# Kernel optimization log

Hardware: AMD Instinct MI355X
Metric: run time of the kernel (lower is better)

The kernel has to match this reference:

```python
import jax, jax.numpy as jnp
import numpy as np

NUM_HEADS = 16
DIM_MODEL = 1024
DIM_K = DIM_MODEL // NUM_HEADS  # 64


def setup_inputs() -> dict:
    key = jax.random.key(0)
    ks = jax.random.split(key, 8)
    B, S, D = 2, 2048, DIM_MODEL
    scale = 1.0 / np.sqrt(D)
    return {
        "X_q": jax.random.normal(ks[0], (B, S, D), dtype=jnp.float32),
        "X_k": jax.random.normal(ks[1], (B, S, D), dtype=jnp.float32),
        "X_v": jax.random.normal(ks[2], (B, S, D), dtype=jnp.float32),
        # weights stored as [in, out] (apply as x @ W)
        "W_query": jax.random.normal(ks[3], (D, D), dtype=jnp.float32) * scale,
        "W_key": jax.random.normal(ks[4], (D, D), dtype=jnp.float32) * scale,
        "W_value": jax.random.normal(ks[5], (D, D), dtype=jnp.float32) * scale,
        "W_hidden": jax.random.normal(ks[6], (D, D), dtype=jnp.float32) * scale,
        "b_hidden": jnp.zeros((D,), dtype=jnp.float32),
    }


def _split_heads(x, B, S):
    # [B, S, D] -> [B, H, S, dk]
    return x.reshape(B, S, NUM_HEADS, DIM_K).transpose(0, 2, 1, 3)


def reference(X_q, X_k, X_v, W_query, W_key, W_value, W_hidden, b_hidden):
    B, S, D = X_q.shape
    Q = _split_heads(X_q @ W_query, B, S)
    K = _split_heads(X_k @ W_key, B, X_k.shape[1])
    V = _split_heads(X_v @ W_value, B, X_v.shape[1])
    Q = Q / np.sqrt(DIM_K).astype(np.float32)
    scores = jnp.einsum("bhqd,bhkd->bhqk", Q, K)
    A = jax.nn.sigmoid(scores)  # sigmoid attention, not softmax
    H = jnp.einsum("bhqk,bhkd->bhqd", A, V)
    # group heads: [B, H, S, dk] -> [B, S, D]
    H_cat = H.transpose(0, 2, 1, 3).reshape(B, S, D)
    H_out = H_cat @ W_hidden + b_hidden
    return (H_out, A)
```

## Files before the change

### kernel.cpp

```cpp
#include <hip/hip_runtime.h>
#include <hip/hip_bf16.h>
#include <cstddef>

typedef __bf16 bf16x8 __attribute__((ext_vector_type(8)));
typedef __bf16 bf16x4 __attribute__((ext_vector_type(4)));
typedef float f32x4 __attribute__((ext_vector_type(4)));

#define MFMA16(a, b, c) __builtin_amdgcn_mfma_f32_16x16x32_bf16((a), (b), (c), 0, 0, 0)

__global__ __launch_bounds__(256) void cvt3(const float* __restrict__ a,
                                            const float* __restrict__ b,
                                            const float* __restrict__ c,
                                            __bf16* __restrict__ oa,
                                            __bf16* __restrict__ ob,
                                            __bf16* __restrict__ oc) {
  const float* src = blockIdx.y == 0 ? a : (blockIdx.y == 1 ? b : c);
  __bf16* dst = blockIdx.y == 0 ? oa : (blockIdx.y == 1 ? ob : oc);
  const size_t i = ((size_t)blockIdx.x * 256 + threadIdx.x) * 4;
  float4 v = *(const float4*)(src + i);
  bf16x4 o = {(__bf16)v.x, (__bf16)v.y, (__bf16)v.z, (__bf16)v.w};
  *(bf16x4*)(dst + i) = o;
}

__global__ __launch_bounds__(256) void twt(const float* __restrict__ w0, const float* __restrict__ w1,
                                           const float* __restrict__ w2, const float* __restrict__ w3,
                                           __bf16* __restrict__ o0, __bf16* __restrict__ o1,
                                           __bf16* __restrict__ o2, __bf16* __restrict__ o3) {
  const float* W;
  __bf16* O;
  switch (blockIdx.z) {
    case 0: W = w0; O = o0; break;
    case 1: W = w1; O = o1; break;
    case 2: W = w2; O = o2; break;
    default: W = w3; O = o3; break;
  }
  __shared__ float t[32][33];
  const int tx = threadIdx.x & 31, ty = threadIdx.x >> 5;
  const int bx = blockIdx.x * 32, by = blockIdx.y * 32;
#pragma unroll
  for (int i = 0; i < 4; ++i)
    t[ty + 8 * i][tx] = W[(size_t)(by + ty + 8 * i) * 1024 + bx + tx];
  __syncthreads();
#pragma unroll
  for (int i = 0; i < 4; ++i)
    O[(size_t)(bx + ty + 8 * i) * 1024 + by + tx] = (__bf16)t[tx][ty + 8 * i];
}

template <bool OUT_BF16>
__device__ __forceinline__ void gemm64_body(const __bf16* __restrict__ A,
                                            const __bf16* __restrict__ B,
                                            void* __restrict__ Cout,
                                            const float* __restrict__ bias,
                                            float scale) {
  constexpr int K = 1024, N = 1024;
  const int tid = threadIdx.x, wave = tid >> 6, lane = tid & 63;
  const int qd = lane >> 4, ln = lane & 15;
  const int m0 = blockIdx.y * 64, n0 = blockIdx.x * 128;
  const int wr = wave & 1, wc = wave >> 1;

  __shared__ __align__(16) __bf16 sA[64][72];
  __shared__ __align__(16) __bf16 sB[128][72];

  f32x4 acc[2][4] = {};

  const int sr = tid >> 2, sc = (tid & 3) * 8;

  for (int k0 = 0; k0 < K; k0 += 64) {
    __syncthreads();
    *(bf16x8*)&sA[sr][sc]      = *(const bf16x8*)(A + (size_t)(m0 + sr) * K + k0 + sc);
    *(bf16x8*)&sA[sr][sc + 32] = *(const bf16x8*)(A + (size_t)(m0 + sr) * K + k0 + sc + 32);
#pragma unroll
    for (int h = 0; h < 128; h += 64)
#pragma unroll
      for (int c = 0; c < 64; c += 32)
        *(bf16x8*)&sB[sr + h][sc + c] =
            *(const bf16x8*)(B + (size_t)(n0 + sr + h) * K + k0 + sc + c);
    __syncthreads();

#pragma unroll
    for (int ks = 0; ks < 64; ks += 32) {
      bf16x8 af[2], bfv[4];
#pragma unroll
      for (int i = 0; i < 2; ++i) af[i] = *(const bf16x8*)&sA[wr * 32 + i * 16 + ln][ks + qd * 8];
#pragma unroll
      for (int j = 0; j < 4; ++j) bfv[j] = *(const bf16x8*)&sB[wc * 64 + j * 16 + ln][ks + qd * 8];
#pragma unroll
      for (int i = 0; i < 2; ++i)
#pragma unroll
        for (int j = 0; j < 4; ++j) acc[i][j] = MFMA16(af[i], bfv[j], acc[i][j]);
    }
  }

#pragma unroll
  for (int i = 0; i < 2; ++i)
#pragma unroll
    for (int j = 0; j < 4; ++j)
#pragma unroll
      for (int r = 0; r < 4; ++r) {
        const int row = m0 + wr * 32 + i * 16 + qd * 4 + r;
        const int col = n0 + wc * 64 + j * 16 + ln;
        float v = acc[i][j][r] * scale;
        if (bias) v += bias[col];
        if (OUT_BF16)
          ((__bf16*)Cout)[(size_t)row * N + col] = (__bf16)v;
        else
          ((float*)Cout)[(size_t)row * N + col] = v;
      }
}

__global__ __launch_bounds__(256) void gemm_qkv(const __bf16* __restrict__ Xq,
                                                const __bf16* __restrict__ Xk,
                                                const __bf16* __restrict__ Xv,
                                                const __bf16* __restrict__ WqT,
                                                const __bf16* __restrict__ WkT,
                                                const __bf16* __restrict__ WvT,
                                                __bf16* __restrict__ Qb,
                                                __bf16* __restrict__ Kb,
                                                __bf16* __restrict__ Vb) {
  const __bf16 *A, *B;
  __bf16* O;
  float sc;
  switch (blockIdx.z) {
    case 0: A = Xq; B = WqT; O = Qb; sc = 0.125f; break;
    case 1: A = Xk; B = WkT; O = Kb; sc = 1.0f; break;
    default: A = Xv; B = WvT; O = Vb; sc = 1.0f; break;
  }
  gemm64_body<true>(A, B, (void*)O, nullptr, sc);
}

__global__ __launch_bounds__(256) void gemm_h(const __bf16* __restrict__ Hc,
                                              const __bf16* __restrict__ WhT,
                                              float* __restrict__ Hout,
                                              const float* __restrict__ bh) {
  gemm64_body<false>(Hc, WhT, (void*)Hout, bh, 1.0f);
}

__global__ __launch_bounds__(256) void attn(const __bf16* __restrict__ Q,
                                            const __bf16* __restrict__ Kb,
                                            const __bf16* __restrict__ Vb,
                                            float* __restrict__ Aout,
                                            __bf16* __restrict__ Hc) {
  const int qt = blockIdx.x, h = blockIdx.y, b = blockIdx.z;
  const int tid = threadIdx.x, wave = tid >> 6, lane = tid & 63;
  const int qd = lane >> 4, ln = lane & 15;
  const int q0 = qt * 64;
  const int wr = wave >> 1, wc = wave & 1;

  __shared__ __align__(16) __bf16 sVt[64][132];
  __shared__ __align__(16) __bf16 sKA[128 * 72];

  const __bf16* Qg = Q + (size_t)(b * 2048 + q0) * 1024 + h * 64;
  bf16x8 qf[2][2];
#pragma unroll
  for (int i = 0; i < 2; ++i)
#pragma unroll
    for (int s = 0; s < 2; ++s)
      qf[i][s] = *(const bf16x8*)(Qg + (size_t)(wr * 32 + i * 16 + ln) * 1024 + s * 32 + qd * 8);

  f32x4 hacc[4] = {};
  float* Ag = Aout + ((size_t)((b * 16 + h) * 2048 + q0)) * 2048;

  for (int kt = 0; kt < 16; ++kt) {
    const int k0 = kt * 128;
    __syncthreads();

    const __bf16* Kg = Kb + (size_t)(b * 2048 + k0) * 1024 + h * 64;
    const __bf16* Vg = Vb + (size_t)(b * 2048 + k0) * 1024 + h * 64;
#pragma unroll
    for (int p = 0; p < 4; ++p) {
      const int idx = p * 256 + tid, row = idx >> 3, ch = (idx & 7) * 8;
      *(bf16x8*)&sKA[row * 72 + ch] = *(const bf16x8*)(Kg + (size_t)row * 1024 + ch);
      bf16x8 v = *(const bf16x8*)(Vg + (size_t)row * 1024 + ch);
#pragma unroll
      for (int e = 0; e < 8; ++e) sVt[ch + e][row] = v[e];
    }
    __syncthreads();

    f32x4 sacc[2][4] = {};
#pragma unroll
    for (int ks = 0; ks < 64; ks += 32) {
      bf16x8 bfv[4];
#pragma unroll
      for (int j = 0; j < 4; ++j)
        bfv[j] = *(const bf16x8*)&sKA[(wc * 64 + j * 16 + ln) * 72 + ks + qd * 8];
#pragma unroll
      for (int i = 0; i < 2; ++i)
#pragma unroll
        for (int j = 0; j < 4; ++j) sacc[i][j] = MFMA16(qf[i][ks / 32], bfv[j], sacc[i][j]);
    }
    __syncthreads();

#pragma unroll
    for (int i = 0; i < 2; ++i)
#pragma unroll
      for (int j = 0; j < 4; ++j)
#pragma unroll
        for (int r = 0; r < 4; ++r) {
          const float s = sacc[i][j][r];
          const float a = 1.0f / (1.0f + __expf(-s));
          const int rr = wr * 32 + i * 16 + qd * 4 + r;
          const int cc = wc * 64 + j * 16 + ln;
          Ag[(size_t)rr * 2048 + k0 + cc] = a;
          sKA[rr * 136 + cc] = (__bf16)a;
        }
    __syncthreads();

#pragma unroll
    for (int ks = 0; ks < 128; ks += 32) {
      bf16x8 pa = *(const bf16x8*)&sKA[(wave * 16 + ln) * 136 + ks + qd * 8];
#pragma unroll
      for (int j = 0; j < 4; ++j) {
        const __bf16* vp = &sVt[j * 16 + ln][ks + qd * 8];
        bf16x4 lo = *(const bf16x4*)vp;
        bf16x4 hi = *(const bf16x4*)(vp + 4);
        bf16x8 bv;
#pragma unroll
        for (int e = 0; e < 4; ++e) { bv[e] = lo[e]; bv[e + 4] = hi[e]; }
        hacc[j] = MFMA16(pa, bv, hacc[j]);
      }
    }
  }

  __bf16* Hg = Hc + (size_t)(b * 2048 + q0) * 1024 + h * 64;
#pragma unroll
  for (int j = 0; j < 4; ++j)
#pragma unroll
    for (int r = 0; r < 4; ++r)
      Hg[(size_t)(wave * 16 + qd * 4 + r) * 1024 + j * 16 + ln] = (__bf16)hacc[j][r];
}

extern "C" void kernel_launch(void* const* d_in, const int* in_sizes, int n_in,
                              void* d_out, int out_size, void* d_ws, size_t ws_size,
                              hipStream_t stream) {
  const float* Xq = (const float*)d_in[0];
  const float* Xk = (const float*)d_in[1];
  const float* Xv = (const float*)d_in[2];
  const float* Wq = (const float*)d_in[3];
  const float* Wk = (const float*)d_in[4];
  const float* Wv = (const float*)d_in[5];
  const float* Wh = (const float*)d_in[6];
  const float* bh = (const float*)d_in[7];

  float* Hout = (float*)d_out;
  float* Aout = Hout + (size_t)4096 * 1024;

  __bf16* p = (__bf16*)d_ws;
  __bf16* Xq_bf = p; p += (size_t)4096 * 1024;
  __bf16* Xk_bf = p; p += (size_t)4096 * 1024;
  __bf16* Xv_bf = p; p += (size_t)4096 * 1024;
  __bf16* WqT = p; p += (size_t)1024 * 1024;
  __bf16* WkT = p; p += (size_t)1024 * 1024;
  __bf16* WvT = p; p += (size_t)1024 * 1024;
  __bf16* WhT = p; p += (size_t)1024 * 1024;
  __bf16* Qb = p; p += (size_t)4096 * 1024;
  __bf16* Kb = p; p += (size_t)4096 * 1024;
  __bf16* Vb = p; p += (size_t)4096 * 1024;
  __bf16* Hc = p; p += (size_t)4096 * 1024;

  cvt3<<<dim3(4096, 3), 256, 0, stream>>>(Xq, Xk, Xv, Xq_bf, Xk_bf, Xv_bf);
  twt<<<dim3(32, 32, 4), 256, 0, stream>>>(Wq, Wk, Wv, Wh, WqT, WkT, WvT, WhT);

  gemm_qkv<<<dim3(8, 64, 3), 256, 0, stream>>>(Xq_bf, Xk_bf, Xv_bf, WqT, WkT, WvT, Qb, Kb, Vb);

  attn<<<dim3(32, 16, 2), 256, 0, stream>>>(Qb, Kb, Vb, Aout, Hc);

  gemm_h<<<dim3(8, 64), 256, 0, stream>>>(Hc, WhT, Hout, bh);
}
```

Baseline: 866.2 us.

## Produce transposed V from GEMM, prefetch K/V into registers, vectorize attention stores

The V projection is now computed as W_v^T·X_v^T, so V comes out transposed and the attention kernel no longer does a scalar element-wise transpose into shared memory. K and V tiles for the next iteration are prefetched into registers while the current tile is computed. The score MFMA operands are swapped so each lane holds four consecutive key columns, which allows float4 nontemporal stores of A and bf16x4 stores of P. Other changes are lighter barriers, rcp-based sigmoid and a 3-blocks-per-CU occupancy hint. In exchange, registers are used for the prefetch buffers and the V GEMM writes with a 4096 stride.

```diff
diff --git a/kernel.cpp b/kernel.cpp
--- a/kernel.cpp
+++ b/kernel.cpp
@@ -7,6 +7,13 @@
 typedef float f32x4 __attribute__((ext_vector_type(4)));
 
 #define MFMA16(a, b, c) __builtin_amdgcn_mfma_f32_16x16x32_bf16((a), (b), (c), 0, 0, 0)
+
+#define LBAR()                                           \
+  do {                                                   \
+    asm volatile("s_waitcnt lgkmcnt(0)" ::: "memory");   \
+    __builtin_amdgcn_s_barrier();                        \
+    __builtin_amdgcn_sched_barrier(0);                   \
+  } while (0)
 
 __global__ __launch_bounds__(256) void cvt3(const float* __restrict__ a,
                                             const float* __restrict__ b,
@@ -51,11 +58,10 @@
                                             const __bf16* __restrict__ B,
                                             void* __restrict__ Cout,
                                             const float* __restrict__ bias,
-                                            float scale) {
-  constexpr int K = 1024, N = 1024;
+                                            float scale, int m0, int n0, int ostride) {
+  constexpr int K = 1024;
   const int tid = threadIdx.x, wave = tid >> 6, lane = tid & 63;
   const int qd = lane >> 4, ln = lane & 15;
-  const int m0 = blockIdx.y * 64, n0 = blockIdx.x * 128;
   const int wr = wave & 1, wc = wave >> 1;
 
   __shared__ __align__(16) __bf16 sA[64][72];
@@ -102,9 +108,9 @@
         float v = acc[i][j][r] * scale;
         if (bias) v += bias[col];
         if (OUT_BF16)
-          ((__bf16*)Cout)[(size_t)row * N + col] = (__bf16)v;
+          ((__bf16*)Cout)[(size_t)row * ostride + col] = (__bf16)v;
         else
-          ((float*)Cout)[(size_t)row * N + col] = v;
+          ((float*)Cout)[(size_t)row * ostride + col] = v;
       }
 }
 
@@ -116,38 +122,39 @@
                                                 const __bf16* __restrict__ WvT,
                                                 __bf16* __restrict__ Qb,
                                                 __bf16* __restrict__ Kb,
-                                                __bf16* __restrict__ Vb) {
-  const __bf16 *A, *B;
-  __bf16* O;
-  float sc;
-  switch (blockIdx.z) {
-    case 0: A = Xq; B = WqT; O = Qb; sc = 0.125f; break;
-    case 1: A = Xk; B = WkT; O = Kb; sc = 1.0f; break;
-    default: A = Xv; B = WvT; O = Vb; sc = 1.0f; break;
-  }
-  gemm64_body<true>(A, B, (void*)O, nullptr, sc);
+                                                __bf16* __restrict__ Vt) {
+  const int z = blockIdx.z;
+  if (z < 2) {
+    gemm64_body<true>(z ? Xk : Xq, z ? WkT : WqT, (void*)(z ? Kb : Qb), nullptr,
+                      z ? 1.0f : 0.125f, blockIdx.y * 64, blockIdx.x * 128, 1024);
+  } else {
+    const int xp = blockIdx.x + (blockIdx.y & 3) * 8;
+    const int yp = blockIdx.y >> 2;
+    gemm64_body<true>(WvT, Xv, (void*)Vt, nullptr, 1.0f, yp * 64, xp * 128, 4096);
+  }
 }
 
 __global__ __launch_bounds__(256) void gemm_h(const __bf16* __restrict__ Hc,
                                               const __bf16* __restrict__ WhT,
                                               float* __restrict__ Hout,
                                               const float* __restrict__ bh) {
-  gemm64_body<false>(Hc, WhT, (void*)Hout, bh, 1.0f);
-}
-
-__global__ __launch_bounds__(256) void attn(const __bf16* __restrict__ Q,
-                                            const __bf16* __restrict__ Kb,
-                                            const __bf16* __restrict__ Vb,
-                                            float* __restrict__ Aout,
-                                            __bf16* __restrict__ Hc) {
+  gemm64_body<false>(Hc, WhT, (void*)Hout, bh, 1.0f, blockIdx.y * 64, blockIdx.x * 128, 1024);
+}
+
+__global__ __launch_bounds__(256, 3) void attn(const __bf16* __restrict__ Q,
+                                               const __bf16* __restrict__ Kb,
+                                               const __bf16* __restrict__ Vt,
+                                               float* __restrict__ Aout,
+                                               __bf16* __restrict__ Hc) {
   const int qt = blockIdx.x, h = blockIdx.y, b = blockIdx.z;
   const int tid = threadIdx.x, wave = tid >> 6, lane = tid & 63;
   const int qd = lane >> 4, ln = lane & 15;
   const int q0 = qt * 64;
   const int wr = wave >> 1, wc = wave & 1;
 
-  __shared__ __align__(16) __bf16 sVt[64][132];
-  __shared__ __align__(16) __bf16 sKA[128 * 72];
+  __shared__ __align__(16) __bf16 sK[128 * 72];
+  __shared__ __align__(16) __bf16 sVt[64 * 136];
+  __bf16* sP = sK;
 
   const __bf16* Qg = Q + (size_t)(b * 2048 + q0) * 1024 + h * 64;
   bf16x8 qf[2][2];
@@ -157,65 +164,80 @@
     for (int s = 0; s < 2; ++s)
       qf[i][s] = *(const bf16x8*)(Qg + (size_t)(wr * 32 + i * 16 + ln) * 1024 + s * 32 + qd * 8);
 
+  const int krow = tid >> 3, kcol = (tid & 7) * 8;
+  const int vrow = tid >> 4, vcol = (tid & 15) * 8;
+  const __bf16* Kg0 = Kb + (size_t)(b * 2048) * 1024 + h * 64;
+  const __bf16* Vg0 = Vt + (size_t)(h * 64) * 4096 + b * 2048;
+
+  bf16x8 kpre[4], vpre[4];
+#pragma unroll
+  for (int p = 0; p < 4; ++p) {
+    kpre[p] = *(const bf16x8*)(Kg0 + (size_t)(p * 32 + krow) * 1024 + kcol);
+    vpre[p] = *(const bf16x8*)(Vg0 + (size_t)(p * 16 + vrow) * 4096 + vcol);
+  }
+
   f32x4 hacc[4] = {};
   float* Ag = Aout + ((size_t)((b * 16 + h) * 2048 + q0)) * 2048;
 
   for (int kt = 0; kt < 16; ++kt) {
     const int k0 = kt * 128;
-    __syncthreads();
-
-    const __bf16* Kg = Kb + (size_t)(b * 2048 + k0) * 1024 + h * 64;
-    const __bf16* Vg = Vb + (size_t)(b * 2048 + k0) * 1024 + h * 64;
+    LBAR();
+
 #pragma unroll
     for (int p = 0; p < 4; ++p) {
-      const int idx = p * 256 + tid, row = idx >> 3, ch = (idx & 7) * 8;
-      *(bf16x8*)&sKA[row * 72 + ch] = *(const bf16x8*)(Kg + (size_t)row * 1024 + ch);
-      bf16x8 v = *(const bf16x8*)(Vg + (size_t)row * 1024 + ch);
-#pragma unroll
-      for (int e = 0; e < 8; ++e) sVt[ch + e][row] = v[e];
-    }
-    __syncthreads();
+      *(bf16x8*)&sK[(p * 32 + krow) * 72 + kcol] = kpre[p];
+      *(bf16x8*)&sVt[(p * 16 + vrow) * 136 + vcol] = vpre[p];
+    }
+    LBAR();
+
+    if (kt < 15) {
+      const int kn = k0 + 128;
+#pragma unroll
+      for (int p = 0; p < 4; ++p) {
+        kpre[p] = *(const bf16x8*)(Kg0 + (size_t)(kn + p * 32 + krow) * 1024 + kcol);
+        vpre[p] = *(const bf16x8*)(Vg0 + (size_t)(p * 16 + vrow) * 4096 + kn + vcol);
+      }
+    }
 
     f32x4 sacc[2][4] = {};
 #pragma unroll
-    for (int ks = 0; ks < 64; ks += 32) {
-      bf16x8 bfv[4];
+    for (int s = 0; s < 2; ++s) {
+      bf16x8 kf[4];
 #pragma unroll
       for (int j = 0; j < 4; ++j)
-        bfv[j] = *(const bf16x8*)&sKA[(wc * 64 + j * 16 + ln) * 72 + ks + qd * 8];
+        kf[j] = *(const bf16x8*)&sK[(wc * 64 + j * 16 + ln) * 72 + s * 32 + qd * 8];
 #pragma unroll
       for (int i = 0; i < 2; ++i)
 #pragma unroll
-        for (int j = 0; j < 4; ++j) sacc[i][j] = MFMA16(qf[i][ks / 32], bfv[j], sacc[i][j]);
-    }
-    __syncthreads();
+        for (int j = 0; j < 4; ++j) sacc[i][j] = MFMA16(kf[j], qf[i][s], sacc[i][j]);
+    }
+    LBAR();
 
 #pragma unroll
     for (int i = 0; i < 2; ++i)
 #pragma unroll
-      for (int j = 0; j < 4; ++j)
+      for (int j = 0; j < 4; ++j) {
+        float a[4];
 #pragma unroll
         for (int r = 0; r < 4; ++r) {
-          const float s = sacc[i][j][r];
-          const float a = 1.0f / (1.0f + __expf(-s));
-          const int rr = wr * 32 + i * 16 + qd * 4 + r;
-          const int cc = wc * 64 + j * 16 + ln;
-          Ag[(size_t)rr * 2048 + k0 + cc] = a;
-          sKA[rr * 136 + cc] = (__bf16)a;
+          const float e = __expf(-sacc[i][j][r]);
+          a[r] = __builtin_amdgcn_rcpf(1.0f + e);
         }
-    __syncthreads();
+        const int qrow = wr * 32 + i * 16 + ln;
+        const int kcol2 = wc * 64 + j * 16 + qd * 4;
+        f32x4 st = {a[0], a[1], a[2], a[3]};
+        __builtin_nontemporal_store(st, (f32x4*)(Ag + (size_t)qrow * 2048 + k0 + kcol2));
+        bf16x4 pb = {(__bf16)a[0], (__bf16)a[1], (__bf16)a[2], (__bf16)a[3]};
+        *(bf16x4*)&sP[qrow * 136 + kcol2] = pb;
+      }
+    LBAR();
 
 #pragma unroll
     for (int ks = 0; ks < 128; ks += 32) {
-      bf16x8 pa = *(const bf16x8*)&sKA[(wave * 16 + ln) * 136 + ks + qd * 8];
+      bf16x8 pa = *(const bf16x8*)&sP[(wave * 16 + ln) * 136 + ks + qd * 8];
 #pragma unroll
       for (int j = 0; j < 4; ++j) {
-        const __bf16* vp = &sVt[j * 16 + ln][ks + qd * 8];
-        bf16x4 lo = *(const bf16x4*)vp;
-        bf16x4 hi = *(const bf16x4*)(vp + 4);
-        bf16x8 bv;
-#pragma unroll
-        for (int e = 0; e < 4; ++e) { bv[e] = lo[e]; bv[e + 4] = hi[e]; }
+        bf16x8 bv = *(const bf16x8*)&sVt[(j * 16 + ln) * 136 + ks + qd * 8];
         hacc[j] = MFMA16(pa, bv, hacc[j]);
       }
     }
@@ -254,15 +276,15 @@
   __bf16* WhT = p; p += (size_t)1024 * 1024;
   __bf16* Qb = p; p += (size_t)4096 * 1024;
   __bf16* Kb = p; p += (size_t)4096 * 1024;
-  __bf16* Vb = p; p += (size_t)4096 * 1024;
+  __bf16* Vt = p; p += (size_t)1024 * 4096;
   __bf16* Hc = p; p += (size_t)4096 * 1024;
 
   cvt3<<<dim3(4096, 3), 256, 0, stream>>>(Xq, Xk, Xv, Xq_bf, Xk_bf, Xv_bf);
   twt<<<dim3(32, 32, 4), 256, 0, stream>>>(Wq, Wk, Wv, Wh, WqT, WkT, WvT, WhT);
 
-  gemm_qkv<<<dim3(8, 64, 3), 256, 0, stream>>>(Xq_bf, Xk_bf, Xv_bf, WqT, WkT, WvT, Qb, Kb, Vb);
-
-  attn<<<dim3(32, 16, 2), 256, 0, stream>>>(Qb, Kb, Vb, Aout, Hc);
+  gemm_qkv<<<dim3(8, 64, 3), 256, 0, stream>>>(Xq_bf, Xk_bf, Xv_bf, WqT, WkT, WvT, Qb, Kb, Vt);
+
+  attn<<<dim3(32, 16, 2), 256, 0, stream>>>(Qb, Kb, Vt, Aout, Hc);
 
   gemm_h<<<dim3(8, 64), 256, 0, stream>>>(Hc, WhT, Hout, bh);
 }
```

Measured after the change: 739.1 us. 1.17x faster.
